# Optimization experiments

Measured on AMD Instinct MI355X. Metric: run time of the kernel, lower is better.

## Reference

```python
import jax, jax.numpy as jnp
import numpy as np

DIM = 768
B, N = 16, 1024
EPS_LN = 1e-5

def _layernorm(x, gamma, beta):
    mu = jnp.mean(x, axis=-1, keepdims=True)
    var = jnp.mean((x - mu) ** 2, axis=-1, keepdims=True)
    return (x - mu) * jax.lax.rsqrt(var + EPS_LN) * gamma + beta

def _gelu(x):
    return jax.nn.gelu(x, approximate=False)

def setup_inputs() -> dict:
    key = jax.random.key(0)
    ks = jax.random.split(key, 10)
    d = DIM
    s1 = 1.0 / np.sqrt(2 * d)
    s = 1.0 / np.sqrt(d)
    return {
        "x": jax.random.normal(ks[0], (B, N, d), dtype=jnp.float32),
        "gamma": jnp.ones((d,), jnp.float32),
        "beta": jnp.zeros((d,), jnp.float32),
        "w1": jax.random.normal(ks[1], (2 * d, d), jnp.float32) * s1,
        "b1": jnp.zeros((d,), jnp.float32),
        "w2": jax.random.normal(ks[2], (d, d), jnp.float32) * s,
        "b2": jnp.zeros((d,), jnp.float32),
        "w3": jax.random.normal(ks[3], (d, d), jnp.float32) * s,
        "b3": jnp.zeros((d,), jnp.float32),
        "w4": jax.random.normal(ks[4], (d, d), jnp.float32) * s,
        "b4": jnp.zeros((d,), jnp.float32),
    }

def reference(x, gamma, beta, w1, b1, w2, b2, w3, b3, w4, b4):
    # x: [B, N, D]
    avg_x = jnp.mean(x, axis=1)                      # [B, D]
    A = avg_x[:, None, :] * jax.nn.sigmoid(_layernorm(x, gamma, beta))  # [B, N, D]
    # batched pairwise Euclidean distance among tokens (replaces python loop)
    sq = jnp.sum(A * A, axis=-1)                     # [B, N]
    d2 = sq[:, :, None] + sq[:, None, :] - 2.0 * jnp.einsum('bnd,bmd->bnm', A, A)
    dist = jnp.sqrt(jnp.clip(d2, 1e-12))             # [B, N, N]
    m = jnp.max(dist, axis=-1)                       # [B, N]
    m_x = x + m[..., None]                           # [B, N, D]
    cat = jnp.concatenate([A, m_x], axis=-1)         # [B, N, 2D]
    m1 = _gelu(cat @ w1 + b1)                        # layer1
    W = _gelu(m1 @ w2 + b2)                          # layer2
    Wdyn = x * W
    l3 = _gelu((m1 * Wdyn) @ w3 + b3)                # layer3
    out = _gelu((x * l3) @ w4 + b4)                  # layer4
    return out.astype(jnp.float32)
```

## Files before the change

kernel.cpp:

```cpp
#include <hip/hip_runtime.h>
#include <hip/hip_fp16.h>
#include <math.h>

#define DIM 768
#define NTOK 1024
#define NBATCH 16
#define BNR (NBATCH * NTOK)

typedef _Float16 f16x8 __attribute__((ext_vector_type(8)));
typedef float f32x4 __attribute__((ext_vector_type(4)));

__device__ __forceinline__ void gl2lds16(const void* g, void* l) {
    __builtin_amdgcn_global_load_lds(
        (const __attribute__((address_space(1))) void*)g,
        (__attribute__((address_space(3))) void*)l, 16, 0, 0);
}

__device__ __forceinline__ float gelu_fast(float z) {
    const float s = z * 0.70710678118654752f;
    const float ax = fabsf(s);
    const float t = __builtin_amdgcn_rcpf(1.0f + 0.3275911f * ax);
    const float poly = t * (0.254829592f + t * (-0.284496736f +
                       t * (1.421413741f + t * (-1.453152027f + t * 1.061405429f))));
    const float e = __expf(-ax * ax);
    float erfv = 1.0f - poly * e;
    erfv = copysignf(erfv, s);
    return 0.5f * z * (1.0f + erfv);
}

__device__ __forceinline__ float block_sum(float v, float* sbuf) {
    #pragma unroll
    for (int o = 32; o > 0; o >>= 1) v += __shfl_down(v, o, 64);
    const int lane = threadIdx.x & 63, w = threadIdx.x >> 6;
    if (lane == 0) sbuf[w] = v;
    __syncthreads();
    const float r = sbuf[0] + sbuf[1] + sbuf[2] + sbuf[3];
    __syncthreads();
    return r;
}

__global__ __launch_bounds__(256) void avg_kernel(const float* __restrict__ x,
                                                  float* __restrict__ avgx) {
    const int d = blockIdx.x * 256 + threadIdx.x;
    const int b = blockIdx.y;
    const int n0 = blockIdx.z * 128;
    const float* xp = x + (size_t)b * NTOK * DIM + (size_t)n0 * DIM + d;
    float s = 0.0f;
    for (int n = 0; n < 128; ++n) s += xp[(size_t)n * DIM];
    atomicAdd(&avgx[b * DIM + d], s * (1.0f / NTOK));
}

__global__ __launch_bounds__(256) void ln_sig_kernel(
    const float* __restrict__ x, const float* __restrict__ gamma,
    const float* __restrict__ beta, const float* __restrict__ avgx,
    __half* __restrict__ Ah, float* __restrict__ sq)
{
    __shared__ float sbuf[4];
    const int row = blockIdx.x;
    const int b = row >> 10;
    const int tid = threadIdx.x;
    const float* xr = x + (size_t)row * DIM;
    float v[3];
    #pragma unroll
    for (int i = 0; i < 3; ++i) v[i] = xr[tid + 256 * i];
    const float mu = block_sum(v[0] + v[1] + v[2], sbuf) * (1.0f / DIM);
    float ss = 0.0f;
    #pragma unroll
    for (int i = 0; i < 3; ++i) { const float d = v[i] - mu; ss += d * d; }
    const float var = block_sum(ss, sbuf) * (1.0f / DIM);
    const float rstd = rsqrtf(var + 1e-5f);
    const float* ag = avgx + b * DIM;
    float qs = 0.0f;
    #pragma unroll
    for (int i = 0; i < 3; ++i) {
        const int d = tid + 256 * i;
        const float ln = (v[i] - mu) * rstd * gamma[d] + beta[d];
        const float sg = 1.0f / (1.0f + expf(-ln));
        const float a = ag[d] * sg;
        const __half h = __float2half(a);
        const float ar = __half2float(h);
        Ah[(size_t)row * DIM + d] = h;
        qs += ar * ar;
    }
    const float tot = block_sum(qs, sbuf);
    if (tid == 0) sq[row] = tot;
}

__global__ __launch_bounds__(256) void wconv(const float* __restrict__ w,
                                             __half* __restrict__ wT, int K, int N)
{
    __shared__ float t[64][65];
    const int k0 = blockIdx.y * 64, n0 = blockIdx.x * 64;
    const int tid = threadIdx.x;
    const int r = tid >> 4, c4 = (tid & 15) * 4;
    #pragma unroll
    for (int p = 0; p < 4; ++p) {
        const int rr = p * 16 + r;
        const float4 v = *(const float4*)&w[(size_t)(k0 + rr) * N + n0 + c4];
        t[rr][c4] = v.x; t[rr][c4 + 1] = v.y; t[rr][c4 + 2] = v.z; t[rr][c4 + 3] = v.w;
    }
    __syncthreads();
    #pragma unroll
    for (int p = 0; p < 4; ++p) {
        const int nn = p * 16 + r;
        ushort4 pk;
        pk.x = __half_as_ushort(__float2half(t[c4 + 0][nn]));
        pk.y = __half_as_ushort(__float2half(t[c4 + 1][nn]));
        pk.z = __half_as_ushort(__float2half(t[c4 + 2][nn]));
        pk.w = __half_as_ushort(__float2half(t[c4 + 3][nn]));
        *(ushort4*)&wT[(size_t)(n0 + nn) * K + k0 + c4] = pk;
    }
}

__global__ __launch_bounds__(256) void xm_kernel(const float* __restrict__ x,
                                                 const float* __restrict__ m,
                                                 __half* __restrict__ xmH) {
    const int row = blockIdx.x;
    const float mv = m[row];
    #pragma unroll
    for (int i = 0; i < 3; ++i) {
        const int d = threadIdx.x + i * 256;
        xmH[(size_t)row * DIM + d] = __float2half(x[(size_t)row * DIM + d] + mv);
    }
}

template<bool CAT, int EPI>
__global__ __launch_bounds__(256, 4) void gemm16(
    const __half* __restrict__ A0, const __half* __restrict__ A1, const int K,
    const __half* __restrict__ BT, const float* __restrict__ bias,
    const float* __restrict__ xin, const __half* __restrict__ m1h,
    __half* __restrict__ outH, float* __restrict__ outF)
{
    __shared__ _Float16 As[128 * 32];
    __shared__ _Float16 Bs[128 * 32];
    const int tid = threadIdx.x;
    const int w = tid >> 6, lane = tid & 63;
    const int wu = __builtin_amdgcn_readfirstlane(w);
    const int wr = w >> 1, wc = w & 1;
    const int R0 = blockIdx.x * 128, J0 = blockIdx.y * 128;
    const int rs = CAT ? DIM : K;
    const int srow = lane >> 2;
    const int sk8 = (((lane & 3) ^ ((lane >> 2) & 3))) * 8;
    const int fx = ((lane >> 4) ^ (lane & 3)) * 8;

    f32x4 acc[4][4];
    #pragma unroll
    for (int mt = 0; mt < 4; ++mt)
        #pragma unroll
        for (int nt = 0; nt < 4; ++nt) {
            f32x4 z = {0.0f, 0.0f, 0.0f, 0.0f};
            acc[mt][nt] = z;
        }

    for (int k0 = 0; k0 < K; k0 += 32) {
        const __half* Ab = (CAT && k0 >= DIM) ? (A1 + (k0 - DIM)) : (A0 + k0);
        #pragma unroll
        for (int i = 0; i < 2; ++i) {
            const int rbase = i * 64 + w * 16;
            const int rbu = i * 64 + wu * 16;
            gl2lds16(Ab + (size_t)(R0 + rbase + srow) * rs + sk8, &As[rbu * 32]);
            gl2lds16(BT + (size_t)(J0 + rbase + srow) * K + k0 + sk8, &Bs[rbu * 32]);
        }
        __syncthreads();
        f16x8 af[4], bf[4];
        #pragma unroll
        for (int mt = 0; mt < 4; ++mt)
            af[mt] = *(const f16x8*)&As[(wr * 64 + mt * 16 + (lane & 15)) * 32 + fx];
        #pragma unroll
        for (int nt = 0; nt < 4; ++nt)
            bf[nt] = *(const f16x8*)&Bs[(wc * 64 + nt * 16 + (lane & 15)) * 32 + fx];
        #pragma unroll
        for (int mt = 0; mt < 4; ++mt)
            #pragma unroll
            for (int nt = 0; nt < 4; ++nt)
                acc[mt][nt] = __builtin_amdgcn_mfma_f32_16x16x32_f16(af[mt], bf[nt], acc[mt][nt], 0, 0, 0);
        __syncthreads();
    }

    #pragma unroll
    for (int mt = 0; mt < 4; ++mt) {
        #pragma unroll
        for (int nt = 0; nt < 4; ++nt) {
            const int col = J0 + wc * 64 + nt * 16 + (lane & 15);
            const float bv = bias[col];
            #pragma unroll
            for (int r = 0; r < 4; ++r) {
                const int row = R0 + wr * 64 + mt * 16 + (lane >> 4) * 4 + r;
                const size_t off = (size_t)row * DIM + col;
                const float g = gelu_fast(acc[mt][nt][r] + bv);
                if (EPI == 0) {
                    outH[off] = __float2half(g);
                } else if (EPI == 1) {
                    outH[off] = __float2half(__half2float(m1h[off]) * xin[off] * g);
                } else if (EPI == 2) {
                    outH[off] = __float2half(xin[off] * g);
                } else {
                    outF[off] = g;
                }
            }
        }
    }
}

__global__ __launch_bounds__(256, 4) void dist16(const __half* __restrict__ Ah,
                                                 const float* __restrict__ sq,
                                                 float* __restrict__ m)
{
    __shared__ _Float16 As[128 * 32];
    __shared__ _Float16 Bs[128 * 32];
    const int tid = threadIdx.x;
    const int w = tid >> 6, lane = tid & 63;
    const int wu = __builtin_amdgcn_readfirstlane(w);
    const int wr = w >> 1, wc = w & 1;
    const int base = blockIdx.x * NTOK;
    const int I0 = blockIdx.y * 128, J0 = blockIdx.z * 128;
    const int srow = lane >> 2;
    const int sk8 = (((lane & 3) ^ ((lane >> 2) & 3))) * 8;
    const int fx = ((lane >> 4) ^ (lane & 3)) * 8;

    f32x4 acc[4][4];
    #pragma unroll
    for (int mt = 0; mt < 4; ++mt)
        #pragma unroll
        for (int nt = 0; nt < 4; ++nt) {
            f32x4 z = {0.0f, 0.0f, 0.0f, 0.0f};
            acc[mt][nt] = z;
        }

    for (int k0 = 0; k0 < DIM; k0 += 32) {
        #pragma unroll
        for (int i = 0; i < 2; ++i) {
            const int rbase = i * 64 + w * 16;
            const int rbu = i * 64 + wu * 16;
            gl2lds16(Ah + (size_t)(base + I0 + rbase + srow) * DIM + k0 + sk8, &As[rbu * 32]);
            gl2lds16(Ah + (size_t)(base + J0 + rbase + srow) * DIM + k0 + sk8, &Bs[rbu * 32]);
        }
        __syncthreads();
        f16x8 af[4], bf[4];
        #pragma unroll
        for (int mt = 0; mt < 4; ++mt)
            af[mt] = *(const f16x8*)&As[(wr * 64 + mt * 16 + (lane & 15)) * 32 + fx];
        #pragma unroll
        for (int nt = 0; nt < 4; ++nt)
            bf[nt] = *(const f16x8*)&Bs[(wc * 64 + nt * 16 + (lane & 15)) * 32 + fx];
        #pragma unroll
        for (int mt = 0; mt < 4; ++mt)
            #pragma unroll
            for (int nt = 0; nt < 4; ++nt)
                acc[mt][nt] = __builtin_amdgcn_mfma_f32_16x16x32_f16(af[mt], bf[nt], acc[mt][nt], 0, 0, 0);
        __syncthreads();
    }

    #pragma unroll
    for (int mt = 0; mt < 4; ++mt) {
        float sqi[4];
        #pragma unroll
        for (int r = 0; r < 4; ++r)
            sqi[r] = sq[base + I0 + wr * 64 + mt * 16 + (lane >> 4) * 4 + r];
        float vmax[4] = {0.0f, 0.0f, 0.0f, 0.0f};
        #pragma unroll
        for (int nt = 0; nt < 4; ++nt) {
            const float sqj = sq[base + J0 + wc * 64 + nt * 16 + (lane & 15)];
            #pragma unroll
            for (int r = 0; r < 4; ++r) {
                const float d2 = sqi[r] + sqj - 2.0f * acc[mt][nt][r];
                vmax[r] = fmaxf(vmax[r], sqrtf(fmaxf(d2, 1e-12f)));
            }
        }
        #pragma unroll
        for (int r = 0; r < 4; ++r) {
            float v = vmax[r];
            v = fmaxf(v, __shfl_xor(v, 1, 64));
            v = fmaxf(v, __shfl_xor(v, 2, 64));
            v = fmaxf(v, __shfl_xor(v, 4, 64));
            v = fmaxf(v, __shfl_xor(v, 8, 64));
            if ((lane & 15) == 0)
                atomicMax((unsigned int*)&m[base + I0 + wr * 64 + mt * 16 + (lane >> 4) * 4 + r],
                          __float_as_uint(v));
        }
    }
}

extern "C" void kernel_launch(void* const* d_in, const int* in_sizes, int n_in,
                              void* d_out, int out_size, void* d_ws, size_t ws_size,
                              hipStream_t stream)
{
    const float* x     = (const float*)d_in[0];
    const float* gamma = (const float*)d_in[1];
    const float* beta  = (const float*)d_in[2];
    const float* w1    = (const float*)d_in[3];
    const float* b1    = (const float*)d_in[4];
    const float* w2    = (const float*)d_in[5];
    const float* b2    = (const float*)d_in[6];
    const float* w3    = (const float*)d_in[7];
    const float* b3    = (const float*)d_in[8];
    const float* w4    = (const float*)d_in[9];
    const float* b4    = (const float*)d_in[10];
    float* out = (float*)d_out;
    float* ws  = (float*)d_ws;

    float* avgx = ws;
    float* sq   = ws + 12288;
    float* mbuf = sq + 16384;
    __half* w1T = (__half*)(mbuf + 16384);
    __half* w2T = w1T + (size_t)1536 * 768;
    __half* w3T = w2T + (size_t)768 * 768;
    __half* w4T = w3T + (size_t)768 * 768;
    __half* P0  = w4T + (size_t)768 * 768;
    __half* P1  = P0 + (size_t)BNR * DIM;
    __half* Ah  = (__half*)d_out;
    __half* xmH = Ah + (size_t)BNR * DIM;

    hipMemsetAsync(avgx, 0, 12288 * sizeof(float), stream);
    hipMemsetAsync(mbuf, 0, BNR * sizeof(float), stream);
    wconv<<<dim3(12, 24), 256, 0, stream>>>(w1, w1T, 1536, 768);
    wconv<<<dim3(12, 12), 256, 0, stream>>>(w2, w2T, 768, 768);
    wconv<<<dim3(12, 12), 256, 0, stream>>>(w3, w3T, 768, 768);
    wconv<<<dim3(12, 12), 256, 0, stream>>>(w4, w4T, 768, 768);
    avg_kernel<<<dim3(3, NBATCH, 8), 256, 0, stream>>>(x, avgx);
    ln_sig_kernel<<<BNR, 256, 0, stream>>>(x, gamma, beta, avgx, Ah, sq);
    dist16<<<dim3(NBATCH, 8, 8), 256, 0, stream>>>(Ah, sq, mbuf);
    xm_kernel<<<BNR, 256, 0, stream>>>(x, mbuf, xmH);
    gemm16<true, 0><<<dim3(128, 6), 256, 0, stream>>>(
        Ah, xmH, 2 * DIM, w1T, b1, nullptr, nullptr, P0, nullptr);
    gemm16<false, 1><<<dim3(128, 6), 256, 0, stream>>>(
        P0, nullptr, DIM, w2T, b2, x, P0, P1, nullptr);
    gemm16<false, 2><<<dim3(128, 6), 256, 0, stream>>>(
        P1, nullptr, DIM, w3T, b3, x, nullptr, P0, nullptr);
    gemm16<false, 3><<<dim3(128, 6), 256, 0, stream>>>(
        P0, nullptr, DIM, w4T, b4, x, nullptr, nullptr, out);
}
```

Baseline: 352.7 us.

## Double-buffer LDS tiles in GEMM and distance kernels, defer sqrt in max

Both MFMA kernels get two LDS buffers: each iteration issues the asynchronous global-to-LDS loads for the next K tile before the MFMAs on the current tile, so load latency overlaps compute and one barrier per iteration is dropped. The GEMM's K becomes a template parameter so the trip count and row stride are compile-time constants and the loop can be partially unrolled. In the distance kernel the row max is taken over squared distances, and the single sqrt is applied only after the shuffle reduction, since sqrt is monotonic. This doubles LDS use per block, which could limit occupancy.

```diff
diff --git a/kernel.cpp b/kernel.cpp
--- a/kernel.cpp
+++ b/kernel.cpp
@@ -124,24 +124,25 @@
     }
 }
 
-template<bool CAT, int EPI>
+template<int K, bool CAT, int EPI>
 __global__ __launch_bounds__(256, 4) void gemm16(
-    const __half* __restrict__ A0, const __half* __restrict__ A1, const int K,
+    const __half* __restrict__ A0, const __half* __restrict__ A1,
     const __half* __restrict__ BT, const float* __restrict__ bias,
     const float* __restrict__ xin, const __half* __restrict__ m1h,
     __half* __restrict__ outH, float* __restrict__ outF)
 {
-    __shared__ _Float16 As[128 * 32];
-    __shared__ _Float16 Bs[128 * 32];
+    __shared__ _Float16 As[2][128 * 32];
+    __shared__ _Float16 Bs[2][128 * 32];
     const int tid = threadIdx.x;
     const int w = tid >> 6, lane = tid & 63;
     const int wu = __builtin_amdgcn_readfirstlane(w);
     const int wr = w >> 1, wc = w & 1;
     const int R0 = blockIdx.x * 128, J0 = blockIdx.y * 128;
-    const int rs = CAT ? DIM : K;
+    constexpr int rs = CAT ? DIM : K;
     const int srow = lane >> 2;
     const int sk8 = (((lane & 3) ^ ((lane >> 2) & 3))) * 8;
     const int fx = ((lane >> 4) ^ (lane & 3)) * 8;
+    constexpr int NT = K / 32;
 
     f32x4 acc[4][4];
     #pragma unroll
@@ -152,23 +153,30 @@
             acc[mt][nt] = z;
         }
 
-    for (int k0 = 0; k0 < K; k0 += 32) {
+    auto stage = [&](int buf, int k0) {
         const __half* Ab = (CAT && k0 >= DIM) ? (A1 + (k0 - DIM)) : (A0 + k0);
         #pragma unroll
         for (int i = 0; i < 2; ++i) {
             const int rbase = i * 64 + w * 16;
             const int rbu = i * 64 + wu * 16;
-            gl2lds16(Ab + (size_t)(R0 + rbase + srow) * rs + sk8, &As[rbu * 32]);
-            gl2lds16(BT + (size_t)(J0 + rbase + srow) * K + k0 + sk8, &Bs[rbu * 32]);
-        }
-        __syncthreads();
+            gl2lds16(Ab + (size_t)(R0 + rbase + srow) * rs + sk8, &As[buf][rbu * 32]);
+            gl2lds16(BT + (size_t)(J0 + rbase + srow) * K + k0 + sk8, &Bs[buf][rbu * 32]);
+        }
+    };
+
+    stage(0, 0);
+    __syncthreads();
+    #pragma unroll 2
+    for (int kt = 0; kt < NT; ++kt) {
+        const int cur = kt & 1;
+        if (kt + 1 < NT) stage(cur ^ 1, (kt + 1) * 32);
         f16x8 af[4], bf[4];
         #pragma unroll
         for (int mt = 0; mt < 4; ++mt)
-            af[mt] = *(const f16x8*)&As[(wr * 64 + mt * 16 + (lane & 15)) * 32 + fx];
+            af[mt] = *(const f16x8*)&As[cur][(wr * 64 + mt * 16 + (lane & 15)) * 32 + fx];
         #pragma unroll
         for (int nt = 0; nt < 4; ++nt)
-            bf[nt] = *(const f16x8*)&Bs[(wc * 64 + nt * 16 + (lane & 15)) * 32 + fx];
+            bf[nt] = *(const f16x8*)&Bs[cur][(wc * 64 + nt * 16 + (lane & 15)) * 32 + fx];
         #pragma unroll
         for (int mt = 0; mt < 4; ++mt)
             #pragma unroll
@@ -206,8 +214,8 @@
                                                  const float* __restrict__ sq,
                                                  float* __restrict__ m)
 {
-    __shared__ _Float16 As[128 * 32];
-    __shared__ _Float16 Bs[128 * 32];
+    __shared__ _Float16 As[2][128 * 32];
+    __shared__ _Float16 Bs[2][128 * 32];
     const int tid = threadIdx.x;
     const int w = tid >> 6, lane = tid & 63;
     const int wu = __builtin_amdgcn_readfirstlane(w);
@@ -217,6 +225,7 @@
     const int srow = lane >> 2;
     const int sk8 = (((lane & 3) ^ ((lane >> 2) & 3))) * 8;
     const int fx = ((lane >> 4) ^ (lane & 3)) * 8;
+    constexpr int NT = DIM / 32;
 
     f32x4 acc[4][4];
     #pragma unroll
@@ -227,22 +236,29 @@
             acc[mt][nt] = z;
         }
 
-    for (int k0 = 0; k0 < DIM; k0 += 32) {
+    auto stage = [&](int buf, int k0) {
         #pragma unroll
         for (int i = 0; i < 2; ++i) {
             const int rbase = i * 64 + w * 16;
             const int rbu = i * 64 + wu * 16;
-            gl2lds16(Ah + (size_t)(base + I0 + rbase + srow) * DIM + k0 + sk8, &As[rbu * 32]);
-            gl2lds16(Ah + (size_t)(base + J0 + rbase + srow) * DIM + k0 + sk8, &Bs[rbu * 32]);
-        }
-        __syncthreads();
+            gl2lds16(Ah + (size_t)(base + I0 + rbase + srow) * DIM + k0 + sk8, &As[buf][rbu * 32]);
+            gl2lds16(Ah + (size_t)(base + J0 + rbase + srow) * DIM + k0 + sk8, &Bs[buf][rbu * 32]);
+        }
+    };
+
+    stage(0, 0);
+    __syncthreads();
+    #pragma unroll 2
+    for (int kt = 0; kt < NT; ++kt) {
+        const int cur = kt & 1;
+        if (kt + 1 < NT) stage(cur ^ 1, (kt + 1) * 32);
         f16x8 af[4], bf[4];
         #pragma unroll
         for (int mt = 0; mt < 4; ++mt)
-            af[mt] = *(const f16x8*)&As[(wr * 64 + mt * 16 + (lane & 15)) * 32 + fx];
+            af[mt] = *(const f16x8*)&As[cur][(wr * 64 + mt * 16 + (lane & 15)) * 32 + fx];
         #pragma unroll
         for (int nt = 0; nt < 4; ++nt)
-            bf[nt] = *(const f16x8*)&Bs[(wc * 64 + nt * 16 + (lane & 15)) * 32 + fx];
+            bf[nt] = *(const f16x8*)&Bs[cur][(wc * 64 + nt * 16 + (lane & 15)) * 32 + fx];
         #pragma unroll
         for (int mt = 0; mt < 4; ++mt)
             #pragma unroll
@@ -257,15 +273,13 @@
         #pragma unroll
         for (int r = 0; r < 4; ++r)
             sqi[r] = sq[base + I0 + wr * 64 + mt * 16 + (lane >> 4) * 4 + r];
-        float vmax[4] = {0.0f, 0.0f, 0.0f, 0.0f};
+        float vmax[4] = {-1e30f, -1e30f, -1e30f, -1e30f};
         #pragma unroll
         for (int nt = 0; nt < 4; ++nt) {
             const float sqj = sq[base + J0 + wc * 64 + nt * 16 + (lane & 15)];
             #pragma unroll
-            for (int r = 0; r < 4; ++r) {
-                const float d2 = sqi[r] + sqj - 2.0f * acc[mt][nt][r];
-                vmax[r] = fmaxf(vmax[r], sqrtf(fmaxf(d2, 1e-12f)));
-            }
+            for (int r = 0; r < 4; ++r)
+                vmax[r] = fmaxf(vmax[r], sqi[r] + sqj - 2.0f * acc[mt][nt][r]);
         }
         #pragma unroll
         for (int r = 0; r < 4; ++r) {
@@ -274,9 +288,11 @@
             v = fmaxf(v, __shfl_xor(v, 2, 64));
             v = fmaxf(v, __shfl_xor(v, 4, 64));
             v = fmaxf(v, __shfl_xor(v, 8, 64));
-            if ((lane & 15) == 0)
+            if ((lane & 15) == 0) {
+                const float d = sqrtf(fmaxf(v, 1e-12f));
                 atomicMax((unsigned int*)&m[base + I0 + wr * 64 + mt * 16 + (lane >> 4) * 4 + r],
-                          __float_as_uint(v));
+                          __float_as_uint(d));
+            }
         }
     }
 }
@@ -321,12 +337,12 @@
     ln_sig_kernel<<<BNR, 256, 0, stream>>>(x, gamma, beta, avgx, Ah, sq);
     dist16<<<dim3(NBATCH, 8, 8), 256, 0, stream>>>(Ah, sq, mbuf);
     xm_kernel<<<BNR, 256, 0, stream>>>(x, mbuf, xmH);
-    gemm16<true, 0><<<dim3(128, 6), 256, 0, stream>>>(
-        Ah, xmH, 2 * DIM, w1T, b1, nullptr, nullptr, P0, nullptr);
-    gemm16<false, 1><<<dim3(128, 6), 256, 0, stream>>>(
-        P0, nullptr, DIM, w2T, b2, x, P0, P1, nullptr);
-    gemm16<false, 2><<<dim3(128, 6), 256, 0, stream>>>(
-        P1, nullptr, DIM, w3T, b3, x, nullptr, P0, nullptr);
-    gemm16<false, 3><<<dim3(128, 6), 256, 0, stream>>>(
-        P0, nullptr, DIM, w4T, b4, x, nullptr, nullptr, out);
-}
+    gemm16<1536, true, 0><<<dim3(128, 6), 256, 0, stream>>>(
+        Ah, xmH, w1T, b1, nullptr, nullptr, P0, nullptr);
+    gemm16<768, false, 1><<<dim3(128, 6), 256, 0, stream>>>(
+        P0, nullptr, w2T, b2, x, P0, P1, nullptr);
+    gemm16<768, false, 2><<<dim3(128, 6), 256, 0, stream>>>(
+        P1, nullptr, w3T, b3, x, nullptr, P0, nullptr);
+    gemm16<768, false, 3><<<dim3(128, 6), 256, 0, stream>>>(
+        P0, nullptr, w4T, b4, x, nullptr, nullptr, out);
+}
```

Result: no change. 350.6 us (-0.6%).
